# Kernel tuning notes

Measured on AMD Instinct MI355X. Metric: run time of the kernel, lower is better.

The kernel has to match this reference:

```python
import jax, jax.numpy as jnp
import numpy as np

B, S, H, DH, E = 8, 2048, 1024, 4096, 8
ALPHA = 0.5
LN_EPS = 1e-5


def setup_inputs() -> dict:
    key = jax.random.key(0)
    ks = jax.random.split(key, 8)
    sc = 0.02
    return {
        "x": jax.random.normal(ks[0], (B, S, H), jnp.float32),
        "We1": jax.random.normal(ks[1], (E, H, DH), jnp.float32) * sc,
        "be1": jnp.zeros((E, DH), jnp.float32),
        "We2": jax.random.normal(ks[2], (E, DH, H), jnp.float32) * sc,
        "be2": jnp.zeros((E, H), jnp.float32),
        "Wq": jax.random.normal(ks[3], (H, H), jnp.float32) * sc,
        "bq": jnp.zeros((H,), jnp.float32),
        "Wk": jax.random.normal(ks[4], (H, H), jnp.float32) * sc,
        "bk": jnp.zeros((H,), jnp.float32),
        "Wv": jax.random.normal(ks[5], (H, H), jnp.float32) * sc,
        "bv": jnp.zeros((H,), jnp.float32),
        "ln_g": jnp.ones((H,), jnp.float32),
        "ln_b": jnp.zeros((H,), jnp.float32),
        "current_expert_idx": E - 1,
    }


def _boosting_forward(x, We1, be1, We2, be2, Wq, bq, Wk, bk, Wv, bv, ln_g, ln_b, cur):
    sg = jax.lax.stop_gradient
    n = cur + 1  # static Python int: number of experts executed
    boost = sg(x)  # boost_input = x.detach()
    outs = []
    for i in range(n):
        h = jax.nn.relu(jnp.einsum("bsh,hf->bsf", boost, We1[i]) + be1[i])
        eo = jnp.einsum("bsf,fh->bsh", h, We2[i]) + be2[i]  # dropout = identity (eval)
        if i < n - 1:
            eo = sg(eo)  # earlier experts detached
        boost = boost + ALPHA * eo
        outs.append(eo)
    stacked = jnp.stack(outs, axis=2)  # [B,S,n,H]
    q = jnp.einsum("bsh,hd->bsd", x, Wq) + bq          # [B,S,H]
    k = jnp.einsum("bseh,hd->bsed", stacked, Wk) + bk  # [B,S,n,H]
    v = jnp.einsum("bseh,hd->bsed", stacked, Wv) + bv
    scores = jnp.einsum("bsd,bsed->bse", q, k) / jnp.sqrt(jnp.asarray(H, x.dtype))
    w = jax.nn.softmax(scores, axis=-1)                # [B,S,n]
    fused = jnp.einsum("bse,bsed->bsd", w, v)          # [B,S,H]
    y = x + fused
    mu = jnp.mean(y, axis=-1, keepdims=True)
    var = jnp.mean(jnp.square(y - mu), axis=-1, keepdims=True)
    return (y - mu) * jax.lax.rsqrt(var + LN_EPS) * ln_g + ln_b


def reference(x, We1, be1, We2, be2, Wq, bq, Wk, bk, Wv, bv, ln_g, ln_b, current_expert_idx):
    return _boosting_forward(x, We1, be1, We2, be2, Wq, bq, Wk, bk, Wv, bv, ln_g, ln_b, int(current_expert_idx))
```

## Files before the change

kernel.cpp:

```cpp
#include <hip/hip_runtime.h>
#include <math.h>

typedef __bf16 bf16_t;
typedef __bf16 bf16x8 __attribute__((ext_vector_type(8)));
typedef __bf16 bf16x4 __attribute__((ext_vector_type(4)));
typedef float f32x4 __attribute__((ext_vector_type(4)));
typedef unsigned int u32;

static constexpr int kBd = 8, kS = 2048, kH = 1024, kDH = 4096, kE = 8;
static constexpr int kM = kBd * kS;
static constexpr float kScale = 0.03125f;

__device__ __forceinline__ void gload_lds16(const void* g, void* l) {
  __builtin_amdgcn_global_load_lds(
      (const __attribute__((address_space(1))) u32*)g,
      (__attribute__((address_space(3))) u32*)l, 16, 0, 0);
}

__global__ __launch_bounds__(256) void cvt_flat_kernel(const float* __restrict__ in,
                                                       bf16_t* __restrict__ out, int n4) {
  int i = blockIdx.x * 256 + threadIdx.x;
  if (i >= n4) return;
  f32x4 v = *(const f32x4*)(in + (size_t)i * 4);
  bf16x4 o;
#pragma unroll
  for (int j = 0; j < 4; ++j) o[j] = (bf16_t)v[j];
  *(bf16x4*)(out + (size_t)i * 4) = o;
}

__global__ __launch_bounds__(256) void transpose_cvt_kernel(
    const float* __restrict__ in, bf16_t* __restrict__ out, int R, int C) {
  __shared__ float tile[32][33];
  int tx = threadIdx.x & 31, ty = threadIdx.x >> 5;
  int c0 = blockIdx.x * 32, r0 = blockIdx.y * 32;
#pragma unroll
  for (int yy = 0; yy < 4; ++yy)
    tile[ty + yy * 8][tx] = in[(size_t)(r0 + ty + yy * 8) * C + c0 + tx];
  __syncthreads();
#pragma unroll
  for (int yy = 0; yy < 4; ++yy)
    out[(size_t)(c0 + ty + yy * 8) * R + r0 + tx] = (bf16_t)tile[tx][ty + yy * 8];
}

template <int MODE>
__global__ __launch_bounds__(512, 2) void gemm256_kernel(
    const bf16_t* __restrict__ A, const bf16_t* __restrict__ Bt,
    int M, int N, int K, int nwg,
    const float* __restrict__ bias,
    bf16_t* __restrict__ outb,
    const float* __restrict__ bin_f, float* __restrict__ bout_f,
    const bf16_t* __restrict__ bin_b, bf16_t* __restrict__ bout_b,
    bf16_t* __restrict__ stacked,
    const float* __restrict__ xres, float* __restrict__ yout,
    const int* __restrict__ curp, int expert_i) {
  if ((MODE == 0 || MODE == 1 || MODE == 4) && expert_i > *curp) return;
  __shared__ char lds_buf[131072];
  char* Ab = lds_buf;
  char* Bb = lds_buf + 65536;
  const int tid = threadIdx.x;
  const int lane = tid & 63, wid = tid >> 6;
  const int wr = wid >> 2, wc = wid & 3;
  const int fr = lane & 15, fh = lane >> 4;
  const int lane_swz = (fr * 64 + fh * 16) ^ ((fr >> 3) << 5);
  const int bid = blockIdx.x;
  const int wg = (bid & 7) * (nwg >> 3) + (bid >> 3);
  const int nMb = M >> 8;
  const int m0 = (wg % nMb) << 8, n0 = (wg / nMb) << 8;
  int grow[2], gcol[2];
#pragma unroll
  for (int j = 0; j < 2; ++j) {
    int L = (j * 512 + tid) * 16;
    int Lp = L ^ (((L >> 9) & 1) << 5);
    int s = Lp >> 10;
    grow[j] = ((s >> 1) << 4) + ((Lp >> 6) & 15);
    gcol[j] = ((s & 1) << 5) + (((Lp >> 4) & 3) << 3);
  }
  const bf16_t* sA[2] = {A + (size_t)(m0 + grow[0]) * K + gcol[0],
                         A + (size_t)(m0 + grow[1]) * K + gcol[1]};
  const bf16_t* sB[2] = {Bt + (size_t)(n0 + grow[0]) * K + gcol[0],
                         Bt + (size_t)(n0 + grow[1]) * K + gcol[1]};
  const size_t rstep = (size_t)128 * K;

#define STAGE(MAT, BASE, tau, h)                                              \
  {                                                                           \
    char* d_ = (BASE) + (((tau) & 1) << 15) + ((h) << 14) + (wid << 10);      \
    gload_lds16(s##MAT[0] + (size_t)(h) * rstep + (tau) * 64, d_);            \
    gload_lds16(s##MAT[1] + (size_t)(h) * rstep + (tau) * 64, d_ + 8192);     \
  }

  const char* Arp = Ab + (wr << 14) + lane_swz;
  const char* Brp = Bb + ((wc >> 1) << 14) + lane_swz;
  const int bq = (wc & 1) * 4;

  f32x4 acc[8][4] = {};
  const int NT = K >> 6;
  STAGE(A, Ab, 0, 0); STAGE(A, Ab, 0, 1);
  STAGE(B, Bb, 0, 0); STAGE(B, Bb, 0, 1);
  STAGE(A, Ab, 1, 0); STAGE(A, Ab, 1, 1);
  asm volatile("s_waitcnt vmcnt(4)" ::: "memory");
  __builtin_amdgcn_s_barrier();

  for (int t = 0; t < NT; ++t) {
    const int bo = (t & 1) << 15;
    const char* Ar = Arp + bo;
    const char* Br = Brp + bo;
    bf16x8 a[4][2], b[4][2];
#pragma unroll
    for (int mf = 0; mf < 4; ++mf)
#pragma unroll
      for (int kk = 0; kk < 2; ++kk)
        a[mf][kk] = *(const bf16x8*)(Ar + (mf * 2 + kk) * 1024);
#pragma unroll
    for (int nf = 0; nf < 4; ++nf)
#pragma unroll
      for (int kk = 0; kk < 2; ++kk)
        b[nf][kk] = *(const bf16x8*)(Br + ((bq + nf) * 2 + kk) * 1024);
    if (t + 1 < NT) STAGE(B, Bb, t + 1, 0);
    __builtin_amdgcn_s_barrier();
    asm volatile("s_waitcnt lgkmcnt(0)" ::: "memory");
    __builtin_amdgcn_sched_barrier(0);
    __builtin_amdgcn_s_setprio(1);
#pragma unroll
    for (int mf = 0; mf < 4; ++mf)
#pragma unroll
      for (int nf = 0; nf < 4; ++nf)
        acc[mf][nf] = __builtin_amdgcn_mfma_f32_16x16x32_bf16(a[mf][0], b[nf][0], acc[mf][nf], 0, 0, 0);
    __builtin_amdgcn_s_setprio(0);
    __builtin_amdgcn_s_barrier();
    if (t + 1 < NT) STAGE(B, Bb, t + 1, 1);
    __builtin_amdgcn_s_barrier();
    __builtin_amdgcn_s_setprio(1);
#pragma unroll
    for (int mf = 0; mf < 4; ++mf)
#pragma unroll
      for (int nf = 0; nf < 4; ++nf)
        acc[mf][nf] = __builtin_amdgcn_mfma_f32_16x16x32_bf16(a[mf][1], b[nf][1], acc[mf][nf], 0, 0, 0);
    __builtin_amdgcn_s_setprio(0);
    __builtin_amdgcn_s_barrier();
#pragma unroll
    for (int mf = 0; mf < 4; ++mf)
#pragma unroll
      for (int kk = 0; kk < 2; ++kk)
        a[mf][kk] = *(const bf16x8*)(Ar + ((mf + 4) * 2 + kk) * 1024);
    __builtin_amdgcn_s_barrier();
    asm volatile("s_waitcnt lgkmcnt(0)" ::: "memory");
    __builtin_amdgcn_sched_barrier(0);
    __builtin_amdgcn_s_setprio(1);
#pragma unroll
    for (int mf = 0; mf < 4; ++mf)
#pragma unroll
      for (int nf = 0; nf < 4; ++nf)
        acc[mf + 4][nf] = __builtin_amdgcn_mfma_f32_16x16x32_bf16(a[mf][0], b[nf][0], acc[mf + 4][nf], 0, 0, 0);
    __builtin_amdgcn_s_setprio(0);
    __builtin_amdgcn_s_barrier();
    if (t + 2 < NT) { STAGE(A, Ab, t + 2, 0); STAGE(A, Ab, t + 2, 1); }
    __builtin_amdgcn_s_setprio(1);
#pragma unroll
    for (int mf = 0; mf < 4; ++mf)
#pragma unroll
      for (int nf = 0; nf < 4; ++nf)
        acc[mf + 4][nf] = __builtin_amdgcn_mfma_f32_16x16x32_bf16(a[mf][1], b[nf][1], acc[mf + 4][nf], 0, 0, 0);
    __builtin_amdgcn_s_setprio(0);
    if (t + 2 < NT) {
      asm volatile("s_waitcnt vmcnt(4)" ::: "memory");
    } else {
      asm volatile("s_waitcnt vmcnt(0)" ::: "memory");
    }
    __builtin_amdgcn_s_barrier();
  }
#undef STAGE

#pragma unroll
  for (int nf = 0; nf < 4; ++nf) {
    const int col = n0 + wc * 64 + nf * 16 + fr;
    const float bv = bias ? bias[col] : 0.0f;
#pragma unroll
    for (int mf = 0; mf < 8; ++mf) {
#pragma unroll
      for (int r = 0; r < 4; ++r) {
        const int row = m0 + wr * 128 + mf * 16 + fh * 4 + r;
        const size_t idx = (size_t)row * N + col;
        float v = acc[mf][nf][r] + bv;
        if (MODE == 0) {
          outb[idx] = (bf16_t)(v > 0.0f ? v : 0.0f);
        } else if (MODE == 2) {
          outb[idx] = (bf16_t)v;
        } else if (MODE == 1) {
          float nb2 = bin_f[idx] + 0.5f * v;
          bout_f[idx] = nb2;
          bout_b[idx] = (bf16_t)nb2;
          stacked[idx] = (bf16_t)v;
        } else if (MODE == 4) {
          float nb2 = (float)bin_b[idx] + 0.5f * v;
          bout_b[idx] = (bf16_t)nb2;
          stacked[idx] = (bf16_t)v;
        } else {
          yout[idx] = v + xres[idx];
        }
      }
    }
  }
}

__global__ __launch_bounds__(256) void scores_mix_kernel(
    const bf16_t* __restrict__ qk, const bf16_t* __restrict__ q,
    const float* __restrict__ bk, const bf16_t* __restrict__ stacked,
    bf16_t* __restrict__ mix, const int* __restrict__ curp) {
  const int n = *curp + 1;
  int lane = threadIdx.x & 63, wave = threadIdx.x >> 6;
  int m = blockIdx.x * 4 + wave;
  size_t base = (size_t)m * kH + lane * 16;
  int c0 = lane * 16;
  bf16x8 qk0 = *(const bf16x8*)(qk + base);
  bf16x8 qk1 = *(const bf16x8*)(qk + base + 8);
  bf16x8 q0 = *(const bf16x8*)(q + base);
  bf16x8 q1 = *(const bf16x8*)(q + base + 8);
  float sc[kE + 1];
  bf16x8 eo0[kE], eo1[kE];
#pragma unroll
  for (int e = 0; e < kE; ++e) {
    sc[e] = 0.0f;
    if (e < n) {
      size_t sb = (size_t)e * kM * kH + base;
      eo0[e] = *(const bf16x8*)(stacked + sb);
      eo1[e] = *(const bf16x8*)(stacked + sb + 8);
      float d = 0.0f;
#pragma unroll
      for (int j = 0; j < 8; ++j)
        d += (float)eo0[e][j] * (float)qk0[j] + (float)eo1[e][j] * (float)qk1[j];
      sc[e] = d;
    }
  }
  {
    float qb = 0.0f;
#pragma unroll
    for (int j = 0; j < 8; ++j)
      qb += (float)q0[j] * bk[c0 + j] + (float)q1[j] * bk[c0 + 8 + j];
    sc[kE] = qb;
  }
#pragma unroll
  for (int off = 32; off >= 1; off >>= 1)
#pragma unroll
    for (int e = 0; e <= kE; ++e) sc[e] += __shfl_xor(sc[e], off, 64);
  float s[kE];
  float mx = -1e30f;
#pragma unroll
  for (int e = 0; e < kE; ++e)
    if (e < n) {
      s[e] = (sc[e] + sc[kE]) * kScale;
      mx = fmaxf(mx, s[e]);
    }
  float Z = 0.0f;
#pragma unroll
  for (int e = 0; e < kE; ++e)
    if (e < n) {
      s[e] = expf(s[e] - mx);
      Z += s[e];
    }
  float inv = 1.0f / Z;
  float mv[16];
#pragma unroll
  for (int j = 0; j < 16; ++j) mv[j] = 0.0f;
#pragma unroll
  for (int e = 0; e < kE; ++e)
    if (e < n) {
      float w = s[e] * inv;
#pragma unroll
      for (int j = 0; j < 8; ++j) {
        mv[j] += w * (float)eo0[e][j];
        mv[8 + j] += w * (float)eo1[e][j];
      }
    }
  bf16x8 o0, o1;
#pragma unroll
  for (int j = 0; j < 8; ++j) {
    o0[j] = (bf16_t)mv[j];
    o1[j] = (bf16_t)mv[8 + j];
  }
  *(bf16x8*)(mix + base) = o0;
  *(bf16x8*)(mix + base + 8) = o1;
}

__global__ __launch_bounds__(256) void layernorm_kernel(
    const float* __restrict__ y, const float* __restrict__ g,
    const float* __restrict__ b, float* __restrict__ out) {
  int lane = threadIdx.x & 63, wave = threadIdx.x >> 6;
  int m = blockIdx.x * 4 + wave;
  size_t base = (size_t)m * kH + lane * 16;
  f32x4 v[4];
#pragma unroll
  for (int j = 0; j < 4; ++j) v[j] = *(const f32x4*)(y + base + j * 4);
  float s = 0.0f, s2 = 0.0f;
#pragma unroll
  for (int j = 0; j < 4; ++j)
#pragma unroll
    for (int t = 0; t < 4; ++t) {
      float u = v[j][t];
      s += u;
      s2 += u * u;
    }
#pragma unroll
  for (int off = 32; off >= 1; off >>= 1) {
    s += __shfl_xor(s, off, 64);
    s2 += __shfl_xor(s2, off, 64);
  }
  float mu = s * (1.0f / kH);
  float var = s2 * (1.0f / kH) - mu * mu;
  float rs = rsqrtf(var + 1e-5f);
  int c0 = lane * 16;
#pragma unroll
  for (int j = 0; j < 4; ++j) {
    f32x4 gg = *(const f32x4*)(g + c0 + j * 4);
    f32x4 bb = *(const f32x4*)(b + c0 + j * 4);
    f32x4 o;
#pragma unroll
    for (int t = 0; t < 4; ++t) o[t] = (v[j][t] - mu) * rs * gg[t] + bb[t];
    *(f32x4*)(out + base + j * 4) = o;
  }
}

extern "C" void kernel_launch(void* const* d_in, const int* in_sizes, int n_in,
                              void* d_out, int out_size, void* d_ws, size_t ws_size,
                              hipStream_t stream) {
  const float* x = (const float*)d_in[0];
  const float* We1 = (const float*)d_in[1];
  const float* be1 = (const float*)d_in[2];
  const float* We2 = (const float*)d_in[3];
  const float* be2 = (const float*)d_in[4];
  const float* Wq = (const float*)d_in[5];
  const float* bq = (const float*)d_in[6];
  const float* Wk = (const float*)d_in[7];
  const float* bk = (const float*)d_in[8];
  const float* Wv = (const float*)d_in[9];
  const float* bv = (const float*)d_in[10];
  const float* ln_g = (const float*)d_in[11];
  const float* ln_b = (const float*)d_in[12];
  const int* curp = (const int*)d_in[13];
  float* out = (float*)d_out;

  char* ws = (char*)d_ws;
  const size_t MB = 1ull << 20;
  bf16_t* stacked = (bf16_t*)(ws);
  bf16_t* xb = (bf16_t*)(ws + 256 * MB);
  bf16_t* boostb = (bf16_t*)(ws + 288 * MB);
  bf16_t* wA = (bf16_t*)(ws + 320 * MB);
  bf16_t* wB = (bf16_t*)(ws + 328 * MB);
  bf16_t* WqT = (bf16_t*)(ws + 336 * MB);
  bf16_t* WkC = (bf16_t*)(ws + 338 * MB);
  bf16_t* WvT = (bf16_t*)(ws + 340 * MB);
  char* dyn = ws + 342 * MB;
  size_t rem = ws_size > 342 * MB ? ws_size - 342 * MB : 0;
  int nchunk;
  bool f32boost;
  if (rem >= 192 * MB) { nchunk = 1; f32boost = true; }
  else if (rem >= 128 * MB) { nchunk = 1; f32boost = false; }
  else if (rem >= 64 * MB) { nchunk = 2; f32boost = false; }
  else { nchunk = 4; f32boost = false; }
  bf16_t* hbuf = (bf16_t*)dyn;
  float* boostf = (float*)(dyn + 128 * MB);
  bf16_t* qb_ = hbuf;
  bf16_t* qkb = boostb;
  bf16_t* mixb = xb;
  float* yf = (float*)ws;

  const int Mc = kM / nchunk;
  const size_t MH = (size_t)kM * kH;
  dim3 blk(256), blk5(512);

  cvt_flat_kernel<<<(kM * kH) / 1024, blk, 0, stream>>>(x, xb, (kM * kH) / 4);
  cvt_flat_kernel<<<(kH * kH) / 1024, blk, 0, stream>>>(Wk, WkC, (kH * kH) / 4);
  transpose_cvt_kernel<<<dim3(kH / 32, kH / 32), blk, 0, stream>>>(Wq, WqT, kH, kH);
  transpose_cvt_kernel<<<dim3(kH / 32, kH / 32), blk, 0, stream>>>(Wv, WvT, kH, kH);

  for (int i = 0; i < kE; ++i) {
    transpose_cvt_kernel<<<dim3(kDH / 32, kH / 32), blk, 0, stream>>>(
        We1 + (size_t)i * kH * kDH, wA, kH, kDH);
    transpose_cvt_kernel<<<dim3(kH / 32, kDH / 32), blk, 0, stream>>>(
        We2 + (size_t)i * kH * kDH, wB, kDH, kH);
    for (int c = 0; c < nchunk; ++c) {
      const size_t ro = (size_t)c * Mc * kH;
      const bf16_t* Ain = ((i == 0) ? xb : boostb) + ro;
      {
        int nwg = (Mc / 256) * (kDH / 256);
        gemm256_kernel<0><<<nwg, blk5, 0, stream>>>(
            Ain, wA, Mc, kDH, kH, nwg, be1 + (size_t)i * kDH, hbuf,
            nullptr, nullptr, nullptr, nullptr, nullptr, nullptr, nullptr, curp, i);
      }
      int nwg = (Mc / 256) * (kH / 256);
      if (f32boost) {
        const float* bin = ((i == 0) ? x : boostf) + ro;
        gemm256_kernel<1><<<nwg, blk5, 0, stream>>>(
            hbuf, wB, Mc, kH, kDH, nwg, be2 + (size_t)i * kH, nullptr,
            bin, boostf + ro, nullptr, boostb + ro, stacked + (size_t)i * MH + ro,
            nullptr, nullptr, curp, i);
      } else {
        const bf16_t* binb = ((i == 0) ? xb : boostb) + ro;
        gemm256_kernel<4><<<nwg, blk5, 0, stream>>>(
            hbuf, wB, Mc, kH, kDH, nwg, be2 + (size_t)i * kH, nullptr,
            nullptr, nullptr, binb, boostb + ro, stacked + (size_t)i * MH + ro,
            nullptr, nullptr, curp, i);
      }
    }
  }

  const int nwgH = (kM / 256) * (kH / 256);
  gemm256_kernel<2><<<nwgH, blk5, 0, stream>>>(
      xb, WqT, kM, kH, kH, nwgH, bq, qb_,
      nullptr, nullptr, nullptr, nullptr, nullptr, nullptr, nullptr, curp, 0);
  gemm256_kernel<2><<<nwgH, blk5, 0, stream>>>(
      qb_, WkC, kM, kH, kH, nwgH, nullptr, qkb,
      nullptr, nullptr, nullptr, nullptr, nullptr, nullptr, nullptr, curp, 0);
  scores_mix_kernel<<<dim3(kM / 4), blk, 0, stream>>>(qkb, qb_, bk, stacked, mixb, curp);
  gemm256_kernel<3><<<nwgH, blk5, 0, stream>>>(
      mixb, WvT, kM, kH, kH, nwgH, bv, nullptr,
      nullptr, nullptr, nullptr, nullptr, nullptr, x, yf, curp, 0);
  layernorm_kernel<<<dim3(kM / 4), blk, 0, stream>>>(yf, ln_g, ln_b, out);
}
```

Measured before the change: 3.142 ms.

## Triple-buffer A tiles in LDS and interleave A reads with MFMA phases

Switches the GEMM to dynamic LDS (160KB) with three A buffers and two B buffers. The main loop becomes four phases, each reading a small slice of A fragments, issuing one global-to-LDS stage, then running a block of MFMAs. The goal is deeper A prefetch and fewer live A registers, so more global-load latency is hidden behind compute. The cost is a larger LDS footprint, which limits residency to one workgroup per CU, and extra barriers per iteration.

```diff
diff --git a/kernel.cpp b/kernel.cpp
--- a/kernel.cpp
+++ b/kernel.cpp
@@ -54,9 +54,9 @@
     const float* __restrict__ xres, float* __restrict__ yout,
     const int* __restrict__ curp, int expert_i) {
   if ((MODE == 0 || MODE == 1 || MODE == 4) && expert_i > *curp) return;
-  __shared__ char lds_buf[131072];
-  char* Ab = lds_buf;
-  char* Bb = lds_buf + 65536;
+  extern __shared__ char lds_buf[];
+  char* Abase = lds_buf;
+  char* Bbase = lds_buf + 98304;
   const int tid = threadIdx.x;
   const int lane = tid & 63, wid = tid >> 6;
   const int wr = wid >> 2, wc = wid & 3;
@@ -81,94 +81,90 @@
                          Bt + (size_t)(n0 + grow[1]) * K + gcol[1]};
   const size_t rstep = (size_t)128 * K;
 
-#define STAGE(MAT, BASE, tau, h)                                              \
+#define STAGE(SP, BASE, tau, h)                                               \
   {                                                                           \
-    char* d_ = (BASE) + (((tau) & 1) << 15) + ((h) << 14) + (wid << 10);      \
-    gload_lds16(s##MAT[0] + (size_t)(h) * rstep + (tau) * 64, d_);            \
-    gload_lds16(s##MAT[1] + (size_t)(h) * rstep + (tau) * 64, d_ + 8192);     \
-  }
-
-  const char* Arp = Ab + (wr << 14) + lane_swz;
-  const char* Brp = Bb + ((wc >> 1) << 14) + lane_swz;
+    char* d_ = (BASE) + ((h) << 14) + (wid << 10);                            \
+    gload_lds16(SP[0] + (size_t)(h)*rstep + (size_t)(tau)*64, d_);            \
+    gload_lds16(SP[1] + (size_t)(h)*rstep + (size_t)(tau)*64, d_ + 8192);     \
+  }
+
+  const int aoff = (wr << 14) + lane_swz;
+  const int boff = ((wc >> 1) << 14) + lane_swz;
   const int bq = (wc & 1) * 4;
 
   f32x4 acc[8][4] = {};
+  bf16x8 b[4][2];
   const int NT = K >> 6;
-  STAGE(A, Ab, 0, 0); STAGE(A, Ab, 0, 1);
-  STAGE(B, Bb, 0, 0); STAGE(B, Bb, 0, 1);
-  STAGE(A, Ab, 1, 0); STAGE(A, Ab, 1, 1);
+  STAGE(sA, Abase, 0, 0); STAGE(sA, Abase, 0, 1);
+  STAGE(sB, Bbase, 0, 0); STAGE(sB, Bbase, 0, 1);
+  STAGE(sA, Abase + 32768, 1, 0); STAGE(sA, Abase + 32768, 1, 1);
   asm volatile("s_waitcnt vmcnt(4)" ::: "memory");
   __builtin_amdgcn_s_barrier();
 
+  int am = 0, am2 = 2;
   for (int t = 0; t < NT; ++t) {
-    const int bo = (t & 1) << 15;
-    const char* Ar = Arp + bo;
-    const char* Br = Brp + bo;
-    bf16x8 a[4][2], b[4][2];
-#pragma unroll
-    for (int mf = 0; mf < 4; ++mf)
-#pragma unroll
-      for (int kk = 0; kk < 2; ++kk)
-        a[mf][kk] = *(const bf16x8*)(Ar + (mf * 2 + kk) * 1024);
+    const char* Ar = Abase + am * 32768 + aoff;
+    const char* Br = Bbase + (t & 1) * 32768 + boff;
+    char* stB = Bbase + ((t + 1) & 1) * 32768;
+    char* stA = Abase + am2 * 32768;
+    bf16x8 a0_, a1_, a2_, a3_;
+
+#define PH_MFMA(p)                                                             \
+  __builtin_amdgcn_s_setprio(1);                                               \
+  _Pragma("unroll") for (int nf = 0; nf < 4; ++nf) {                           \
+    acc[2 * (p)][nf] =                                                         \
+        __builtin_amdgcn_mfma_f32_16x16x32_bf16(a0_, b[nf][0], acc[2 * (p)][nf], 0, 0, 0); \
+    acc[2 * (p)][nf] =                                                         \
+        __builtin_amdgcn_mfma_f32_16x16x32_bf16(a1_, b[nf][1], acc[2 * (p)][nf], 0, 0, 0); \
+    acc[2 * (p) + 1][nf] =                                                     \
+        __builtin_amdgcn_mfma_f32_16x16x32_bf16(a2_, b[nf][0], acc[2 * (p) + 1][nf], 0, 0, 0); \
+    acc[2 * (p) + 1][nf] =                                                     \
+        __builtin_amdgcn_mfma_f32_16x16x32_bf16(a3_, b[nf][1], acc[2 * (p) + 1][nf], 0, 0, 0); \
+  }                                                                            \
+  __builtin_amdgcn_s_setprio(0);
+
+#define RD_A(p)                                                                \
+  a0_ = *(const bf16x8*)(Ar + ((2 * (p)) * 2 + 0) * 1024);                     \
+  a1_ = *(const bf16x8*)(Ar + ((2 * (p)) * 2 + 1) * 1024);                     \
+  a2_ = *(const bf16x8*)(Ar + ((2 * (p) + 1) * 2 + 0) * 1024);                 \
+  a3_ = *(const bf16x8*)(Ar + ((2 * (p) + 1) * 2 + 1) * 1024);
+
 #pragma unroll
     for (int nf = 0; nf < 4; ++nf)
 #pragma unroll
       for (int kk = 0; kk < 2; ++kk)
         b[nf][kk] = *(const bf16x8*)(Br + ((bq + nf) * 2 + kk) * 1024);
-    if (t + 1 < NT) STAGE(B, Bb, t + 1, 0);
-    __builtin_amdgcn_s_barrier();
-    asm volatile("s_waitcnt lgkmcnt(0)" ::: "memory");
-    __builtin_amdgcn_sched_barrier(0);
-    __builtin_amdgcn_s_setprio(1);
-#pragma unroll
-    for (int mf = 0; mf < 4; ++mf)
-#pragma unroll
-      for (int nf = 0; nf < 4; ++nf)
-        acc[mf][nf] = __builtin_amdgcn_mfma_f32_16x16x32_bf16(a[mf][0], b[nf][0], acc[mf][nf], 0, 0, 0);
-    __builtin_amdgcn_s_setprio(0);
-    __builtin_amdgcn_s_barrier();
-    if (t + 1 < NT) STAGE(B, Bb, t + 1, 1);
-    __builtin_amdgcn_s_barrier();
-    __builtin_amdgcn_s_setprio(1);
-#pragma unroll
-    for (int mf = 0; mf < 4; ++mf)
-#pragma unroll
-      for (int nf = 0; nf < 4; ++nf)
-        acc[mf][nf] = __builtin_amdgcn_mfma_f32_16x16x32_bf16(a[mf][1], b[nf][1], acc[mf][nf], 0, 0, 0);
-    __builtin_amdgcn_s_setprio(0);
-    __builtin_amdgcn_s_barrier();
-#pragma unroll
-    for (int mf = 0; mf < 4; ++mf)
-#pragma unroll
-      for (int kk = 0; kk < 2; ++kk)
-        a[mf][kk] = *(const bf16x8*)(Ar + ((mf + 4) * 2 + kk) * 1024);
-    __builtin_amdgcn_s_barrier();
-    asm volatile("s_waitcnt lgkmcnt(0)" ::: "memory");
-    __builtin_amdgcn_sched_barrier(0);
-    __builtin_amdgcn_s_setprio(1);
-#pragma unroll
-    for (int mf = 0; mf < 4; ++mf)
-#pragma unroll
-      for (int nf = 0; nf < 4; ++nf)
-        acc[mf + 4][nf] = __builtin_amdgcn_mfma_f32_16x16x32_bf16(a[mf][0], b[nf][0], acc[mf + 4][nf], 0, 0, 0);
-    __builtin_amdgcn_s_setprio(0);
-    __builtin_amdgcn_s_barrier();
-    if (t + 2 < NT) { STAGE(A, Ab, t + 2, 0); STAGE(A, Ab, t + 2, 1); }
-    __builtin_amdgcn_s_setprio(1);
-#pragma unroll
-    for (int mf = 0; mf < 4; ++mf)
-#pragma unroll
-      for (int nf = 0; nf < 4; ++nf)
-        acc[mf + 4][nf] = __builtin_amdgcn_mfma_f32_16x16x32_bf16(a[mf][1], b[nf][1], acc[mf + 4][nf], 0, 0, 0);
-    __builtin_amdgcn_s_setprio(0);
+    RD_A(0);
+    if (t + 1 < NT) STAGE(sB, stB, t + 1, 0);
+    __builtin_amdgcn_s_barrier();
+    PH_MFMA(0);
+    __builtin_amdgcn_s_barrier();
+    RD_A(1);
+    if (t + 1 < NT) STAGE(sB, stB, t + 1, 1);
+    __builtin_amdgcn_s_barrier();
+    PH_MFMA(1);
+    __builtin_amdgcn_s_barrier();
+    RD_A(2);
+    if (t + 2 < NT) STAGE(sA, stA, t + 2, 0);
+    __builtin_amdgcn_s_barrier();
+    PH_MFMA(2);
+    __builtin_amdgcn_s_barrier();
+    RD_A(3);
+    if (t + 2 < NT) STAGE(sA, stA, t + 2, 1);
+    __builtin_amdgcn_s_barrier();
+    PH_MFMA(3);
     if (t + 2 < NT) {
       asm volatile("s_waitcnt vmcnt(4)" ::: "memory");
     } else {
       asm volatile("s_waitcnt vmcnt(0)" ::: "memory");
     }
     __builtin_amdgcn_s_barrier();
+    am = (am == 2) ? 0 : am + 1;
+    am2 = (am2 == 2) ? 0 : am2 + 1;
   }
 #undef STAGE
+#undef PH_MFMA
+#undef RD_A
 
 #pragma unroll
   for (int nf = 0; nf < 4; ++nf) {
@@ -365,6 +361,7 @@
 
   const int Mc = kM / nchunk;
   const size_t MH = (size_t)kM * kH;
+  const u32 kLds = 163840;
   dim3 blk(256), blk5(512);
 
   cvt_flat_kernel<<<(kM * kH) / 1024, blk, 0, stream>>>(x, xb, (kM * kH) / 4);
@@ -382,20 +379,20 @@
       const bf16_t* Ain = ((i == 0) ? xb : boostb) + ro;
       {
         int nwg = (Mc / 256) * (kDH / 256);
-        gemm256_kernel<0><<<nwg, blk5, 0, stream>>>(
+        gemm256_kernel<0><<<nwg, blk5, kLds, stream>>>(
             Ain, wA, Mc, kDH, kH, nwg, be1 + (size_t)i * kDH, hbuf,
             nullptr, nullptr, nullptr, nullptr, nullptr, nullptr, nullptr, curp, i);
       }
       int nwg = (Mc / 256) * (kH / 256);
       if (f32boost) {
         const float* bin = ((i == 0) ? x : boostf) + ro;
-        gemm256_kernel<1><<<nwg, blk5, 0, stream>>>(
+        gemm256_kernel<1><<<nwg, blk5, kLds, stream>>>(
             hbuf, wB, Mc, kH, kDH, nwg, be2 + (size_t)i * kH, nullptr,
             bin, boostf + ro, nullptr, boostb + ro, stacked + (size_t)i * MH + ro,
             nullptr, nullptr, curp, i);
       } else {
         const bf16_t* binb = ((i == 0) ? xb : boostb) + ro;
-        gemm256_kernel<4><<<nwg, blk5, 0, stream>>>(
+        gemm256_kernel<4><<<nwg, blk5, kLds, stream>>>(
             hbuf, wB, Mc, kH, kDH, nwg, be2 + (size_t)i * kH, nullptr,
             nullptr, nullptr, binb, boostb + ro, stacked + (size_t)i * MH + ro,
             nullptr, nullptr, curp, i);
@@ -404,14 +401,14 @@
   }
 
   const int nwgH = (kM / 256) * (kH / 256);
-  gemm256_kernel<2><<<nwgH, blk5, 0, stream>>>(
+  gemm256_kernel<2><<<nwgH, blk5, kLds, stream>>>(
       xb, WqT, kM, kH, kH, nwgH, bq, qb_,
       nullptr, nullptr, nullptr, nullptr, nullptr, nullptr, nullptr, curp, 0);
-  gemm256_kernel<2><<<nwgH, blk5, 0, stream>>>(
+  gemm256_kernel<2><<<nwgH, blk5, kLds, stream>>>(
       qb_, WkC, kM, kH, kH, nwgH, nullptr, qkb,
       nullptr, nullptr, nullptr, nullptr, nullptr, nullptr, nullptr, curp, 0);
   scores_mix_kernel<<<dim3(kM / 4), blk, 0, stream>>>(qkb, qb_, bk, stacked, mixb, curp);
-  gemm256_kernel<3><<<nwgH, blk5, 0, stream>>>(
+  gemm256_kernel<3><<<nwgH, blk5, kLds, stream>>>(
       mixb, WvT, kM, kH, kH, nwgH, bv, nullptr,
       nullptr, nullptr, nullptr, nullptr, nullptr, x, yf, curp, 0);
   layernorm_kernel<<<dim3(kM / 4), blk, 0, stream>>>(yf, ln_g, ln_b, out);
```

Result: no change. 3.162 ms (+0.6%).
